# Kernel optimization log

Hardware: AMD Instinct MI355X
Metric: run time of the kernel (lower is better)

The kernel has to match this reference:

```python
import jax, jax.numpy as jnp
import numpy as np

N = 100_000          # nodes
E = 1_600_000        # edges (avg degree 16)
IN_C, OUT_C = 256, 128


def setup_inputs() -> dict:
    key = jax.random.key(0)
    k1, k2, k3, k4, k5 = jax.random.split(key, 5)
    X = jax.random.normal(k1, (N, IN_C), dtype=jnp.float32)
    # nn.Linear(in, out, bias=False) weight has shape [out, in]
    W = jax.random.normal(k2, (OUT_C, IN_C), dtype=jnp.float32) * (1.0 / np.sqrt(IN_C))
    A_rows = jnp.sort(jax.random.randint(k3, (E,), 0, N, dtype=jnp.int32))
    A_cols = jax.random.randint(k4, (E,), 0, N, dtype=jnp.int32)
    # positive values mimicking symmetric-normalized adjacency entries
    A_vals = jax.random.uniform(k5, (E,), dtype=jnp.float32) * (1.0 / 16.0)
    return {"X": X, "W": W, "A_rows": A_rows, "A_cols": A_cols, "A_vals": A_vals}


def reference(X, W, A_rows, A_cols, A_vals):
    # X = self._linear(X)  ->  X @ W^T   [N, OUT_C]
    H = jnp.einsum("ni,oi->no", X, W)
    # X = torch.sparse.mm(A_hat, X): out[r] += v * H[c] for each edge (r, c, v)
    msgs = A_vals[:, None] * H[A_cols]                      # [E, OUT_C]
    out = jax.ops.segment_sum(msgs, A_rows, num_segments=N)  # [N, OUT_C]
    return out
```

## Files before the change

kernel.cpp:

```cpp
#include <hip/hip_runtime.h>
#include <hip/hip_bf16.h>

#define NNODES 100000
#define NEDGES 1600000
#define IN_C   256
#define OUT_C  128

typedef short bf16x8 __attribute__((ext_vector_type(8)));
typedef float f32x4  __attribute__((ext_vector_type(4)));

static __device__ __forceinline__ unsigned short f2bf(float f) {
    union { float f; unsigned u; } c; c.f = f;
    unsigned r = c.u + 0x7fffu + ((c.u >> 16) & 1u);
    return (unsigned short)(r >> 16);
}

union BF8 { bf16x8 v; unsigned short s[8]; };

__global__ __launch_bounds__(512, 4) void gemm_xwt(const float* __restrict__ X,
                                                   const float* __restrict__ W,
                                                   signed char* __restrict__ H8,
                                                   float* __restrict__ scale) {
    __shared__ unsigned short Wsh[128 * 256];

    const int tid  = threadIdx.x;
    const int lane = tid & 63;
    const int wid  = tid >> 6;

#pragma unroll
    for (int p = 0; p < 16; ++p) {
        int idx = p * 512 + tid;
        int n   = idx >> 6;
        int c4  = idx & 63;
        float4 v = *(const float4*)(W + (size_t)n * IN_C + c4 * 4);
        int byte = (n * 512 + c4 * 8) ^ ((n & 7) << 4);
        *(ushort4*)((char*)Wsh + byte) =
            make_ushort4(f2bf(v.x), f2bf(v.y), f2bf(v.z), f2bf(v.w));
    }
    __syncthreads();

    const int r0   = blockIdx.x * 128 + wid * 16;
    int arow = r0 + (lane & 15);
    if (arow > NNODES - 1) arow = NNODES - 1;
    const float* xrow = X + (size_t)arow * IN_C + (lane >> 4) * 8;

    f32x4 acc[8] = {};
#pragma unroll
    for (int ks = 0; ks < 8; ++ks) {
        float4 a0 = *(const float4*)(xrow + ks * 32);
        float4 a1 = *(const float4*)(xrow + ks * 32 + 4);
        BF8 t;
        t.s[0] = f2bf(a0.x); t.s[1] = f2bf(a0.y); t.s[2] = f2bf(a0.z); t.s[3] = f2bf(a0.w);
        t.s[4] = f2bf(a1.x); t.s[5] = f2bf(a1.y); t.s[6] = f2bf(a1.z); t.s[7] = f2bf(a1.w);
        const int kb = ks * 64 + (lane >> 4) * 16;
#pragma unroll
        for (int n8 = 0; n8 < 8; ++n8) {
            int nr   = n8 * 16 + (lane & 15);
            int byte = (nr * 512 + kb) ^ ((nr & 7) << 4);
            bf16x8 b = *(const bf16x8*)((const char*)Wsh + byte);
            acc[n8] = __builtin_amdgcn_mfma_f32_16x16x32_bf16(t.v, b, acc[n8],
                                                              0, 0, 0);
        }
    }

    float amax[4];
#pragma unroll
    for (int r = 0; r < 4; ++r) {
        float m = 0.f;
#pragma unroll
        for (int n8 = 0; n8 < 8; ++n8) m = fmaxf(m, fabsf(acc[n8][r]));
        amax[r] = m;
    }
#pragma unroll
    for (int d = 1; d < 16; d <<= 1)
#pragma unroll
        for (int r = 0; r < 4; ++r)
            amax[r] = fmaxf(amax[r], __shfl_xor(amax[r], d));

#pragma unroll
    for (int r = 0; r < 4; ++r) {
        int grow = r0 + (lane >> 4) * 4 + r;
        if (grow < NNODES) {
            float am  = amax[r];
            float inv = am > 0.f ? 127.f / am : 0.f;
            if ((lane & 15) == 0) scale[grow] = am * (1.f / 127.f);
#pragma unroll
            for (int n8 = 0; n8 < 8; ++n8) {
                float q = rintf(acc[n8][r] * inv);
                q = fminf(127.f, fmaxf(-127.f, q));
                H8[(size_t)grow * OUT_C + n8 * 16 + (lane & 15)] = (signed char)q;
            }
        }
    }
}

__global__ __launch_bounds__(256) void build_rowptr(const int* __restrict__ rows,
                                                    int* __restrict__ rowptr) {
    int r = blockIdx.x * 256 + threadIdx.x;
    if (r > NNODES) return;
    int lo = 0, hi = NEDGES;
    while (lo < hi) {
        int mid = (lo + hi) >> 1;
        if (rows[mid] < r) lo = mid + 1; else hi = mid;
    }
    rowptr[r] = lo;
}

__global__ __launch_bounds__(256) void spmm_rows(const uint2* __restrict__ H2,
                                                 const int* __restrict__ rowptr,
                                                 const int* __restrict__ cols,
                                                 const float* __restrict__ vals,
                                                 const float* __restrict__ scale,
                                                 float* __restrict__ out) {
    const int wid  = threadIdx.x >> 6;
    const int lane = threadIdx.x & 63;
    const int row  = blockIdx.x * 4 + wid;
    if (row >= NNODES) return;

    const int s  = rowptr[row];
    const int e  = rowptr[row + 1];
    const int g  = lane >> 4;
    const int cg = lane & 15;

    float acc[8];
#pragma unroll
    for (int t = 0; t < 8; ++t) acc[t] = 0.f;

    for (int base = s; base < e; base += 64) {
        const int cnt = (e - base < 64) ? (e - base) : 64;
        int   ec = 0;
        float ev = 0.f;
        if (lane < cnt) {
            ec = cols[base + lane];
            ev = vals[base + lane] * scale[ec];
        }

        int j = 0;
        for (; j + 16 <= cnt; j += 16) {
#pragma unroll
            for (int q = 0; q < 4; ++q) {
                int   c = __shfl(ec, j + q * 4 + g);
                float v = __shfl(ev, j + q * 4 + g);
                uint2 u = H2[(size_t)c * 16 + cg];
                acc[0] += v * (float)(signed char)(u.x);
                acc[1] += v * (float)(signed char)(u.x >> 8);
                acc[2] += v * (float)(signed char)(u.x >> 16);
                acc[3] += v * (float)(signed char)(u.x >> 24);
                acc[4] += v * (float)(signed char)(u.y);
                acc[5] += v * (float)(signed char)(u.y >> 8);
                acc[6] += v * (float)(signed char)(u.y >> 16);
                acc[7] += v * (float)(signed char)(u.y >> 24);
            }
        }
        for (; j < cnt; j += 4) {
            int   c = __shfl(ec, j + g);
            float v = __shfl(ev, j + g);
            uint2 u = H2[(size_t)c * 16 + cg];
            acc[0] += v * (float)(signed char)(u.x);
            acc[1] += v * (float)(signed char)(u.x >> 8);
            acc[2] += v * (float)(signed char)(u.x >> 16);
            acc[3] += v * (float)(signed char)(u.x >> 24);
            acc[4] += v * (float)(signed char)(u.y);
            acc[5] += v * (float)(signed char)(u.y >> 8);
            acc[6] += v * (float)(signed char)(u.y >> 16);
            acc[7] += v * (float)(signed char)(u.y >> 24);
        }
    }

#pragma unroll
    for (int t = 0; t < 8; ++t) {
        acc[t] += __shfl_xor(acc[t], 16);
        acc[t] += __shfl_xor(acc[t], 32);
    }
    if (lane < 16) {
        f32x4 v0 = { acc[0], acc[1], acc[2], acc[3] };
        f32x4 v1 = { acc[4], acc[5], acc[6], acc[7] };
        __builtin_nontemporal_store(v0, (f32x4*)(out + (size_t)row * OUT_C + cg * 8));
        __builtin_nontemporal_store(v1, (f32x4*)(out + (size_t)row * OUT_C + cg * 8 + 4));
    }
}

extern "C" void kernel_launch(void* const* d_in, const int* in_sizes, int n_in,
                              void* d_out, int out_size, void* d_ws, size_t ws_size,
                              hipStream_t stream) {
    const float* X      = (const float*)d_in[0];
    const float* W      = (const float*)d_in[1];
    const int*   A_rows = (const int*)d_in[2];
    const int*   A_cols = (const int*)d_in[3];
    const float* A_vals = (const float*)d_in[4];
    float* out = (float*)d_out;

    signed char* H8    = (signed char*)d_ws;
    float*       scale = (float*)((char*)d_ws + (size_t)NNODES * OUT_C);
    int*         rowptr = (int*)((char*)scale + (size_t)NNODES * sizeof(float));

    gemm_xwt<<<(NNODES + 127) / 128, 512, 0, stream>>>(X, W, H8, scale);
    build_rowptr<<<(NNODES + 1 + 255) / 256, 256, 0, stream>>>(A_rows, rowptr);
    spmm_rows<<<(NNODES + 3) / 4, 256, 0, stream>>>((const uint2*)H8, rowptr,
                                                    A_cols, A_vals, scale, out);
}
```

Baseline: 92.15 us.

## Split quantized features into column slabs and process one row per thread

H8 is stored as four column slabs of 32 bytes per node, and values are offset to unsigned by adding 128. The SpMM now gives each thread one row of one slab. Each edge costs two 16-byte gathers, and the offset is removed at the end using the sum of the edge weights. Each slab is 3.2 MB, so it may fit in cache. The change also drops the wave-level shuffles. The cost is redundant reads of cols, vals and scale (once per slab), 32 accumulators per thread, and load imbalance across threads for rows of different degree.

```diff
diff --git a/kernel.cpp b/kernel.cpp
--- a/kernel.cpp
+++ b/kernel.cpp
@@ -5,6 +5,7 @@
 #define NEDGES 1600000
 #define IN_C   256
 #define OUT_C  128
+#define NSLAB  4
 
 typedef short bf16x8 __attribute__((ext_vector_type(8)));
 typedef float f32x4  __attribute__((ext_vector_type(4)));
@@ -19,7 +20,7 @@
 
 __global__ __launch_bounds__(512, 4) void gemm_xwt(const float* __restrict__ X,
                                                    const float* __restrict__ W,
-                                                   signed char* __restrict__ H8,
+                                                   unsigned char* __restrict__ H8,
                                                    float* __restrict__ scale) {
     __shared__ unsigned short Wsh[128 * 256];
 
@@ -88,7 +89,9 @@
             for (int n8 = 0; n8 < 8; ++n8) {
                 float q = rintf(acc[n8][r] * inv);
                 q = fminf(127.f, fmaxf(-127.f, q));
-                H8[(size_t)grow * OUT_C + n8 * 16 + (lane & 15)] = (signed char)q;
+                size_t off = (size_t)(n8 >> 1) * (NNODES * 32)
+                           + (size_t)grow * 32 + (n8 & 1) * 16 + (lane & 15);
+                H8[off] = (unsigned char)((int)q + 128);
             }
         }
     }
@@ -106,77 +109,62 @@
     rowptr[r] = lo;
 }
 
-__global__ __launch_bounds__(256) void spmm_rows(const uint2* __restrict__ H2,
+__global__ __launch_bounds__(256) void spmm_rows(const unsigned char* __restrict__ H8,
                                                  const int* __restrict__ rowptr,
                                                  const int* __restrict__ cols,
                                                  const float* __restrict__ vals,
                                                  const float* __restrict__ scale,
                                                  float* __restrict__ out) {
-    const int wid  = threadIdx.x >> 6;
-    const int lane = threadIdx.x & 63;
-    const int row  = blockIdx.x * 4 + wid;
+    const int b     = blockIdx.x;
+    const int slab  = (b & 7) >> 1;
+    const int chunk = (b >> 3) * 2 + (b & 1);
+    const int row   = chunk * 256 + threadIdx.x;
     if (row >= NNODES) return;
 
-    const int s  = rowptr[row];
-    const int e  = rowptr[row + 1];
-    const int g  = lane >> 4;
-    const int cg = lane & 15;
+    const unsigned char* Hs = H8 + (size_t)slab * (NNODES * 32);
 
-    float acc[8];
+    const int s = rowptr[row];
+    const int e = rowptr[row + 1];
+
+    float acc[32];
 #pragma unroll
-    for (int t = 0; t < 8; ++t) acc[t] = 0.f;
+    for (int t = 0; t < 32; ++t) acc[t] = 0.f;
+    float sw = 0.f;
 
-    for (int base = s; base < e; base += 64) {
-        const int cnt = (e - base < 64) ? (e - base) : 64;
-        int   ec = 0;
-        float ev = 0.f;
-        if (lane < cnt) {
-            ec = cols[base + lane];
-            ev = vals[base + lane] * scale[ec];
+#pragma unroll 2
+    for (int i = s; i < e; ++i) {
+        int   c = cols[i];
+        float w = vals[i] * scale[c];
+        const uint4* hp = (const uint4*)(Hs + (size_t)c * 32);
+        uint4 u0 = hp[0];
+        uint4 u1 = hp[1];
+        sw += w;
+#pragma unroll
+        for (int d = 0; d < 4; ++d) {
+            unsigned ud = (&u0.x)[d];
+            acc[d * 4 + 0] += w * (float)( ud        & 0xffu);
+            acc[d * 4 + 1] += w * (float)((ud >>  8) & 0xffu);
+            acc[d * 4 + 2] += w * (float)((ud >> 16) & 0xffu);
+            acc[d * 4 + 3] += w * (float)( ud >> 24);
         }
-
-        int j = 0;
-        for (; j + 16 <= cnt; j += 16) {
 #pragma unroll
-            for (int q = 0; q < 4; ++q) {
-                int   c = __shfl(ec, j + q * 4 + g);
-                float v = __shfl(ev, j + q * 4 + g);
-                uint2 u = H2[(size_t)c * 16 + cg];
-                acc[0] += v * (float)(signed char)(u.x);
-                acc[1] += v * (float)(signed char)(u.x >> 8);
-                acc[2] += v * (float)(signed char)(u.x >> 16);
-                acc[3] += v * (float)(signed char)(u.x >> 24);
-                acc[4] += v * (float)(signed char)(u.y);
-                acc[5] += v * (float)(signed char)(u.y >> 8);
-                acc[6] += v * (float)(signed char)(u.y >> 16);
-                acc[7] += v * (float)(signed char)(u.y >> 24);
-            }
-        }
-        for (; j < cnt; j += 4) {
-            int   c = __shfl(ec, j + g);
-            float v = __shfl(ev, j + g);
-            uint2 u = H2[(size_t)c * 16 + cg];
-            acc[0] += v * (float)(signed char)(u.x);
-            acc[1] += v * (float)(signed char)(u.x >> 8);
-            acc[2] += v * (float)(signed char)(u.x >> 16);
-            acc[3] += v * (float)(signed char)(u.x >> 24);
-            acc[4] += v * (float)(signed char)(u.y);
-            acc[5] += v * (float)(signed char)(u.y >> 8);
-            acc[6] += v * (float)(signed char)(u.y >> 16);
-            acc[7] += v * (float)(signed char)(u.y >> 24);
+        for (int d = 0; d < 4; ++d) {
+            unsigned ud = (&u1.x)[d];
+            acc[16 + d * 4 + 0] += w * (float)( ud        & 0xffu);
+            acc[16 + d * 4 + 1] += w * (float)((ud >>  8) & 0xffu);
+            acc[16 + d * 4 + 2] += w * (float)((ud >> 16) & 0xffu);
+            acc[16 + d * 4 + 3] += w * (float)( ud >> 24);
         }
     }
 
+    float* orow = out + (size_t)row * OUT_C + slab * 32;
 #pragma unroll
     for (int t = 0; t < 8; ++t) {
-        acc[t] += __shfl_xor(acc[t], 16);
-        acc[t] += __shfl_xor(acc[t], 32);
-    }
-    if (lane < 16) {
-        f32x4 v0 = { acc[0], acc[1], acc[2], acc[3] };
-        f32x4 v1 = { acc[4], acc[5], acc[6], acc[7] };
-        __builtin_nontemporal_store(v0, (f32x4*)(out + (size_t)row * OUT_C + cg * 8));
-        __builtin_nontemporal_store(v1, (f32x4*)(out + (size_t)row * OUT_C + cg * 8 + 4));
+        f32x4 v = { acc[t * 4 + 0] - 128.f * sw,
+                    acc[t * 4 + 1] - 128.f * sw,
+                    acc[t * 4 + 2] - 128.f * sw,
+                    acc[t * 4 + 3] - 128.f * sw };
+        __builtin_nontemporal_store(v, (f32x4*)(orow + t * 4));
     }
 }
 
@@ -190,12 +178,11 @@
     const float* A_vals = (const float*)d_in[4];
     float* out = (float*)d_out;
 
-    signed char* H8    = (signed char*)d_ws;
-    float*       scale = (float*)((char*)d_ws + (size_t)NNODES * OUT_C);
-    int*         rowptr = (int*)((char*)scale + (size_t)NNODES * sizeof(float));
+    unsigned char* H8    = (unsigned char*)d_ws;
+    float*         scale = (float*)((char*)d_ws + (size_t)NNODES * OUT_C);
+    int*           rowptr = (int*)((char*)scale + (size_t)NNODES * sizeof(float));
 
     gemm_xwt<<<(NNODES + 127) / 128, 512, 0, stream>>>(X, W, H8, scale);
     build_rowptr<<<(NNODES + 1 + 255) / 256, 256, 0, stream>>>(A_rows, rowptr);
-    spmm_rows<<<(NNODES + 3) / 4, 256, 0, stream>>>((const uint2*)H8, rowptr,
-                                                    A_cols, A_vals, scale, out);
+    spmm_rows<<<8 * 196, 256, 0, stream>>>(H8, rowptr, A_cols, A_vals, scale, out);
 }
```

Result: slower. 202.4 us (+119.7%).
